# Kernel tuning notes

Hardware: AMD Instinct MI355X
Metric: run time of the kernel (lower is better)

The kernel has to match this reference:

```python
import jax, jax.numpy as jnp
import numpy as np

B, N, E, H, L = 1, 1024, 32, 1024, 8  # batch, num concepts, dim_edge, dim_hidden, stack_len


def setup_inputs() -> dict:
    key = jax.random.key(0)
    k = jax.random.split(key, 12)
    vision_feat = jax.random.normal(k[0], (B, 36, H), jnp.float32)   # unused by forward
    feat = jax.random.normal(k[1], (B, N - 1, N, E), jnp.float32)
    feat_edge = jax.random.normal(k[2], (B, 1, N, E), jnp.float32)
    c_i = jax.random.normal(k[3], (B, H), jnp.float32)
    relation_mask = jnp.ones((B, N), jnp.float32)                    # only its size is read
    att_stack = jax.random.uniform(k[4], (B, N, N, L), dtype=jnp.float32)
    sp = jax.random.uniform(k[5], (B, L), dtype=jnp.float32)
    stack_ptr = sp / jnp.sum(sp, axis=-1, keepdims=True)             # soft stack pointer
    mem_in = jax.random.normal(k[6], (B, H), jnp.float32)
    mono_mask = (jax.random.uniform(k[7], (B, N, N, 1)) > 0.5).astype(jnp.float32)
    cross_mask = jax.random.uniform(k[8], (E,), dtype=jnp.float32)
    w_c = jax.random.normal(k[9], (E, H), jnp.float32) / np.sqrt(H).astype(np.float32)
    b_c = jax.random.normal(k[10], (E,), jnp.float32) * 0.01
    return {"vision_feat": vision_feat, "feat": feat, "feat_edge": feat_edge,
            "c_i": c_i, "relation_mask": relation_mask, "att_stack": att_stack,
            "stack_ptr": stack_ptr, "mem_in": mem_in, "mono_mask": mono_mask,
            "cross_mask": cross_mask, "w_c": w_c, "b_c": b_c}


def reference(vision_feat, feat, feat_edge, c_i, relation_mask, att_stack,
              stack_ptr, mem_in, mono_mask, cross_mask, w_c, b_c):
    b = feat_edge.shape[0]
    # query = map_c(c_i).view(B,1,1,-1).expand_as(feat_edge)
    query = (c_i @ w_c.T + b_c).reshape(b, 1, 1, -1)
    query = jnp.broadcast_to(query, feat_edge.shape)                 # (B,1,N,E)
    I = jnp.concatenate([query, feat], axis=1)                       # (B,N,N,E)
    # Fusion: -(x-y)^2 + relu(x+y), feat_edge broadcasts over dim1
    elt_prod = -(I - feat_edge) ** 2 + jax.nn.relu(I + feat_edge)    # (B,N,N,E)
    weit_matrix = mono_mask * elt_prod                               # (B,N,N,E)
    # soft stack read + permute(0,2,1): att_in[b,y,x] = sum_l att_stack[b,x,y,l]*ptr[b,l]
    att_in = jnp.einsum('bxyl,bl->byx', att_stack, stack_ptr)        # (B,N,N)
    # (att_in @ weit_matrix) @ cross_mask, then permute(0,2,1).
    # Contract the edge dim first (mathematically identical by linearity).
    wv = jnp.einsum('bmye,e->bmy', weit_matrix, cross_mask)          # (B,N,N)
    att_out = jnp.einsum('bxy,bmy->bxm', att_in, wv)                 # (B,N,N)
    # max-normalize with detached norm clamped to >= 1
    norm = jax.lax.stop_gradient(jnp.max(att_out, axis=1, keepdims=True))
    norm = jnp.where(norm <= 1, jnp.ones_like(norm), norm)
    att_out = att_out / norm
    # soft stack write
    ptr = stack_ptr[:, None, None, :]                                # (B,1,1,L)
    att_stack_new = att_out[..., None] * ptr + att_stack * (1 - ptr) # (B,N,N,L)
    return att_stack_new, stack_ptr, jnp.zeros_like(mem_in)
```

## Files before the change

kernel.cpp:

```cpp
#include <hip/hip_runtime.h>
#include <math.h>

#define N 1024
#define E 32
#define L 8
#define NN ((size_t)N * N)

using short8 = __attribute__((ext_vector_type(8))) short;
using f32x4v = __attribute__((ext_vector_type(4))) float;

__device__ inline ushort2 split_bf16(float v) {
  unsigned ui = __float_as_uint(v);
  ushort h = (ushort)(ui >> 16);
  float hv = __uint_as_float((unsigned)h << 16);
  float r = v - hv;
  ushort l = (ushort)(__float_as_uint(r) >> 16);
  return make_ushort2(h, l);
}

__device__ inline void gload16(const void* g, void* l) {
  __builtin_amdgcn_global_load_lds(
      (const __attribute__((address_space(1))) unsigned int*)g,
      (__attribute__((address_space(3))) unsigned int*)l, 16, 0, 0);
}

__global__ __launch_bounds__(256) void k_wv(
    const float* __restrict__ feat, const float* __restrict__ fe,
    const float* __restrict__ mono, const float* __restrict__ cm,
    const float* __restrict__ c_i, const float* __restrict__ w_c,
    const float* __restrict__ b_c,
    ushort* __restrict__ wv_h, ushort* __restrict__ wv_l) {
  __shared__ __align__(16) float qsm[32];
  int tid = threadIdx.x;
  int b = blockIdx.x;
  int seg = tid & 7;
  int rl = tid >> 3;
  bool qblock = (b < 8);
  if (qblock) {
    int e = tid >> 3, r = tid & 7;
    float s = 0.f;
    for (int h = r; h < N; h += 8) s += c_i[h] * w_c[e * N + h];
    s += __shfl_down(s, 4, 8);
    s += __shfl_down(s, 2, 8);
    s += __shfl_down(s, 1, 8);
    if (r == 0) qsm[e] = s + b_c[e];
    __syncthreads();
  }
  float4 c = *(const float4*)(cm + seg * 4);
  float4 qa;
  if (qblock) qa = *((const float4*)qsm + seg);
  #pragma unroll
  for (int it = 0; it < 4; ++it) {
    int gid = b * 128 + it * 32 + rl;
    int m = gid >> 10;
    int y = gid & (N - 1);
    float4 a;
    if (qblock) {
      a = qa;
    } else {
      a = *(const float4*)(feat + ((size_t)(m - 1) * N + y) * E + seg * 4);
    }
    float4 f = *(const float4*)(fe + (size_t)y * E + seg * 4);
    float dx = a.x - f.x, dy = a.y - f.y, dz = a.z - f.z, dw = a.w - f.w;
    float s = c.x * (fmaxf(a.x + f.x, 0.f) - dx * dx)
            + c.y * (fmaxf(a.y + f.y, 0.f) - dy * dy)
            + c.z * (fmaxf(a.z + f.z, 0.f) - dz * dz)
            + c.w * (fmaxf(a.w + f.w, 0.f) - dw * dw);
    s += __shfl_down(s, 4, 8);
    s += __shfl_down(s, 2, 8);
    s += __shfl_down(s, 1, 8);
    if (seg == 0) {
      float v = mono[gid] * s;
      ushort2 hl = split_bf16(v);
      wv_h[gid] = hl.x;
      wv_l[gid] = hl.y;
    }
  }
}

__global__ __launch_bounds__(256) void k_P(
    const float* __restrict__ att_stack, const float* __restrict__ ptr,
    ushort* __restrict__ Pt_h, ushort* __restrict__ Pt_l,
    float* __restrict__ out_tail) {
  __shared__ ushort Ts[2][64][66];
  int tid = threadIdx.x;
  int b = blockIdx.x;
  if (b < 256) {
    int j0 = (b >> 4) * 64;
    int i0 = (b & 15) * 64;
    float p0 = ptr[0], p1 = ptr[1], p2 = ptr[2], p3 = ptr[3];
    float p4 = ptr[4], p5 = ptr[5], p6 = ptr[6], p7 = ptr[7];
    int w = tid >> 6, lane = tid & 63;
    #pragma unroll 4
    for (int r = 0; r < 16; ++r) {
      int jl = r * 4 + w;
      int il = lane;
      const float4* a =
          (const float4*)(att_stack + ((size_t)(j0 + jl) * N + i0 + il) * L);
      float4 a0 = a[0], a1 = a[1];
      float s = a0.x * p0 + a0.y * p1 + a0.z * p2 + a0.w * p3
              + a1.x * p4 + a1.y * p5 + a1.z * p6 + a1.w * p7;
      ushort2 hl = split_bf16(s);
      Ts[0][il][jl] = hl.x;
      Ts[1][il][jl] = hl.y;
    }
    __syncthreads();
    int il = tid >> 2, cc = tid & 3;
    size_t o = (size_t)(i0 + il) * N + j0 + cc * 16;
    {
      const uint* sp = (const uint*)&Ts[0][il][cc * 16];
      uint4 d0 = {sp[0], sp[1], sp[2], sp[3]};
      uint4 d1 = {sp[4], sp[5], sp[6], sp[7]};
      *(uint4*)&Pt_h[o] = d0;
      *(uint4*)&Pt_h[o + 8] = d1;
    }
    {
      const uint* sp = (const uint*)&Ts[1][il][cc * 16];
      uint4 d0 = {sp[0], sp[1], sp[2], sp[3]};
      uint4 d1 = {sp[4], sp[5], sp[6], sp[7]};
      *(uint4*)&Pt_l[o] = d0;
      *(uint4*)&Pt_l[o + 8] = d1;
    }
  } else {
    if (tid < 8) out_tail[tid] = ptr[tid];
    for (int i = tid; i < N; i += 256) out_tail[8 + i] = 0.f;
  }
}

__global__ __launch_bounds__(256) void k_mm(
    const ushort* __restrict__ Pt_h, const ushort* __restrict__ Pt_l,
    const ushort* __restrict__ wv_h, const ushort* __restrict__ wv_l,
    float* __restrict__ C, float* __restrict__ normp) {
  __shared__ ushort As[2][64][32];
  __shared__ ushort Bs[2][64][32];
  __shared__ float nm[64][17];
  int tid = threadIdx.x;
  int lane = tid & 63, w = tid >> 6;
  int x0 = blockIdx.x * 64, m0 = blockIdx.y * 64;
  int srow = w * 16 + (lane >> 2);
  int scol = (lane & 3) * 8;
  const ushort* gAh = Pt_h + (size_t)(x0 + srow) * N + scol;
  const ushort* gAl = Pt_l + (size_t)(x0 + srow) * N + scol;
  const ushort* gBh = wv_h + (size_t)(m0 + srow) * N + scol;
  const ushort* gBl = wv_l + (size_t)(m0 + srow) * N + scol;
  ushort* lAh = &As[0][w * 16][0];
  ushort* lAl = &As[1][w * 16][0];
  ushort* lBh = &Bs[0][w * 16][0];
  ushort* lBl = &Bs[1][w * 16][0];
  int fr = w * 16 + (lane & 15);
  int fk = (lane >> 4) * 8;
  int fn = lane & 15;
  f32x4v acc[4];
  #pragma unroll
  for (int t = 0; t < 4; ++t) acc[t] = (f32x4v){0.f, 0.f, 0.f, 0.f};
  for (int kt = 0; kt < 32; ++kt) {
    __syncthreads();
    gload16(gAh + kt * 32, lAh);
    gload16(gAl + kt * 32, lAl);
    gload16(gBh + kt * 32, lBh);
    gload16(gBl + kt * 32, lBl);
    __syncthreads();
    short8 Ah = *(const short8*)&As[0][fr][fk];
    short8 Al = *(const short8*)&As[1][fr][fk];
    #pragma unroll
    for (int t = 0; t < 4; ++t) {
      short8 Bh = *(const short8*)&Bs[0][t * 16 + fn][fk];
      short8 Bl = *(const short8*)&Bs[1][t * 16 + fn][fk];
      acc[t] = __builtin_amdgcn_mfma_f32_16x16x32_bf16(Ah, Bh, acc[t], 0, 0, 0);
      acc[t] = __builtin_amdgcn_mfma_f32_16x16x32_bf16(Ah, Bl, acc[t], 0, 0, 0);
      acc[t] = __builtin_amdgcn_mfma_f32_16x16x32_bf16(Al, Bh, acc[t], 0, 0, 0);
    }
  }
  int orow = x0 + w * 16 + (lane >> 4) * 4;
  int ocol = m0 + fn;
  int cidx = w * 4 + (lane >> 4);
  #pragma unroll
  for (int t = 0; t < 4; ++t) {
    float mx = -INFINITY;
    #pragma unroll
    for (int r = 0; r < 4; ++r) {
      float v = acc[t][r];
      C[(size_t)(orow + r) * N + ocol + t * 16] = v;
      mx = fmaxf(mx, v);
    }
    nm[t * 16 + fn][cidx] = mx;
  }
  __syncthreads();
  if (tid < 64) {
    float mx = nm[tid][0];
    #pragma unroll
    for (int j = 1; j < 16; ++j) mx = fmaxf(mx, nm[tid][j]);
    normp[(size_t)blockIdx.x * N + m0 + tid] = mx;
  }
}

__global__ __launch_bounds__(256) void k_norm2(
    const float* __restrict__ normp, float* __restrict__ norm) {
  int m = blockIdx.x * 256 + threadIdx.x;
  float mx = normp[m];
  #pragma unroll
  for (int xg = 1; xg < 16; ++xg)
    mx = fmaxf(mx, normp[(size_t)xg * N + m]);
  norm[m] = (mx <= 1.f) ? 1.f : mx;
}

__global__ __launch_bounds__(256) void k_blend(
    const float* __restrict__ C, const float* __restrict__ norm,
    const float* __restrict__ att_stack, const float* __restrict__ ptr,
    float* __restrict__ out) {
  int gid = blockIdx.x * 256 + threadIdx.x;
  int m = gid & (N - 1);
  float a = C[gid] / norm[m];
  const float4* s = (const float4*)(att_stack + (size_t)gid * L);
  float4 s0 = s[0], s1 = s[1];
  float p0 = ptr[0], p1 = ptr[1], p2 = ptr[2], p3 = ptr[3];
  float p4 = ptr[4], p5 = ptr[5], p6 = ptr[6], p7 = ptr[7];
  float4 o0, o1;
  o0.x = a * p0 + s0.x * (1.f - p0);
  o0.y = a * p1 + s0.y * (1.f - p1);
  o0.z = a * p2 + s0.z * (1.f - p2);
  o0.w = a * p3 + s0.w * (1.f - p3);
  o1.x = a * p4 + s1.x * (1.f - p4);
  o1.y = a * p5 + s1.y * (1.f - p5);
  o1.z = a * p6 + s1.z * (1.f - p6);
  o1.w = a * p7 + s1.w * (1.f - p7);
  float4* o = (float4*)(out + (size_t)gid * L);
  o[0] = o0;
  o[1] = o1;
}

extern "C" void kernel_launch(void* const* d_in, const int* in_sizes, int n_in,
                              void* d_out, int out_size, void* d_ws, size_t ws_size,
                              hipStream_t stream) {
  const float* feat      = (const float*)d_in[1];
  const float* feat_edge = (const float*)d_in[2];
  const float* c_i       = (const float*)d_in[3];
  const float* att_stack = (const float*)d_in[5];
  const float* stack_ptr = (const float*)d_in[6];
  const float* mono_mask = (const float*)d_in[8];
  const float* cross_mask= (const float*)d_in[9];
  const float* w_c       = (const float*)d_in[10];
  const float* b_c       = (const float*)d_in[11];

  float* out = (float*)d_out;

  ushort* wv_h = (ushort*)d_ws;
  ushort* wv_l = wv_h + NN;
  ushort* Pt_h = wv_l + NN;
  ushort* Pt_l = Pt_h + NN;
  float*  C    = (float*)(Pt_l + NN);
  float*  normp= C + NN;
  float*  norm = normp + (size_t)16 * N;

  float* out_tail = out + NN * L;

  k_wv<<<8192, 256, 0, stream>>>(feat, feat_edge, mono_mask, cross_mask,
                                 c_i, w_c, b_c, wv_h, wv_l);
  k_P<<<257, 256, 0, stream>>>(att_stack, stack_ptr, Pt_h, Pt_l, out_tail);
  dim3 mmgrid(16, 16);
  k_mm<<<mmgrid, 256, 0, stream>>>(Pt_h, Pt_l, wv_h, wv_l, C, normp);
  k_norm2<<<4, 256, 0, stream>>>(normp, norm);
  k_blend<<<4096, 256, 0, stream>>>(C, norm, att_stack, stack_ptr, out);
}
```

Before: 292.1 us.

## Merge prep kernels, double-buffer and swizzle GEMM LDS, fold norm into blend

Result: faster. 280.3 us (-4.0%).

```diff
diff --git a/kernel.cpp b/kernel.cpp
--- a/kernel.cpp
+++ b/kernel.cpp
@@ -24,70 +24,67 @@
       (__attribute__((address_space(3))) unsigned int*)l, 16, 0, 0);
 }
 
-__global__ __launch_bounds__(256) void k_wv(
+__global__ __launch_bounds__(256) void k_prep(
     const float* __restrict__ feat, const float* __restrict__ fe,
     const float* __restrict__ mono, const float* __restrict__ cm,
     const float* __restrict__ c_i, const float* __restrict__ w_c,
     const float* __restrict__ b_c,
-    ushort* __restrict__ wv_h, ushort* __restrict__ wv_l) {
-  __shared__ __align__(16) float qsm[32];
-  int tid = threadIdx.x;
-  int b = blockIdx.x;
-  int seg = tid & 7;
-  int rl = tid >> 3;
-  bool qblock = (b < 8);
-  if (qblock) {
-    int e = tid >> 3, r = tid & 7;
-    float s = 0.f;
-    for (int h = r; h < N; h += 8) s += c_i[h] * w_c[e * N + h];
-    s += __shfl_down(s, 4, 8);
-    s += __shfl_down(s, 2, 8);
-    s += __shfl_down(s, 1, 8);
-    if (r == 0) qsm[e] = s + b_c[e];
-    __syncthreads();
-  }
-  float4 c = *(const float4*)(cm + seg * 4);
-  float4 qa;
-  if (qblock) qa = *((const float4*)qsm + seg);
-  #pragma unroll
-  for (int it = 0; it < 4; ++it) {
-    int gid = b * 128 + it * 32 + rl;
-    int m = gid >> 10;
-    int y = gid & (N - 1);
-    float4 a;
-    if (qblock) {
-      a = qa;
-    } else {
-      a = *(const float4*)(feat + ((size_t)(m - 1) * N + y) * E + seg * 4);
-    }
-    float4 f = *(const float4*)(fe + (size_t)y * E + seg * 4);
-    float dx = a.x - f.x, dy = a.y - f.y, dz = a.z - f.z, dw = a.w - f.w;
-    float s = c.x * (fmaxf(a.x + f.x, 0.f) - dx * dx)
-            + c.y * (fmaxf(a.y + f.y, 0.f) - dy * dy)
-            + c.z * (fmaxf(a.z + f.z, 0.f) - dz * dz)
-            + c.w * (fmaxf(a.w + f.w, 0.f) - dw * dw);
-    s += __shfl_down(s, 4, 8);
-    s += __shfl_down(s, 2, 8);
-    s += __shfl_down(s, 1, 8);
-    if (seg == 0) {
-      float v = mono[gid] * s;
-      ushort2 hl = split_bf16(v);
-      wv_h[gid] = hl.x;
-      wv_l[gid] = hl.y;
-    }
-  }
-}
-
-__global__ __launch_bounds__(256) void k_P(
     const float* __restrict__ att_stack, const float* __restrict__ ptr,
+    ushort* __restrict__ wv_h, ushort* __restrict__ wv_l,
     ushort* __restrict__ Pt_h, ushort* __restrict__ Pt_l,
     float* __restrict__ out_tail) {
+  __shared__ __align__(16) float qsm[32];
   __shared__ ushort Ts[2][64][66];
   int tid = threadIdx.x;
   int b = blockIdx.x;
-  if (b < 256) {
-    int j0 = (b >> 4) * 64;
-    int i0 = (b & 15) * 64;
+  if (b < 8192) {
+    int seg = tid & 7;
+    int rl = tid >> 3;
+    bool qblock = (b < 8);
+    if (qblock) {
+      int e = tid >> 3, r = tid & 7;
+      float s = 0.f;
+      for (int h = r; h < N; h += 8) s += c_i[h] * w_c[e * N + h];
+      s += __shfl_down(s, 4, 8);
+      s += __shfl_down(s, 2, 8);
+      s += __shfl_down(s, 1, 8);
+      if (r == 0) qsm[e] = s + b_c[e];
+      __syncthreads();
+    }
+    float4 c = *(const float4*)(cm + seg * 4);
+    float4 qa;
+    if (qblock) qa = *((const float4*)qsm + seg);
+    #pragma unroll
+    for (int it = 0; it < 4; ++it) {
+      int gid = b * 128 + it * 32 + rl;
+      int m = gid >> 10;
+      int y = gid & (N - 1);
+      float4 a;
+      if (qblock) {
+        a = qa;
+      } else {
+        a = *(const float4*)(feat + ((size_t)(m - 1) * N + y) * E + seg * 4);
+      }
+      float4 f = *(const float4*)(fe + (size_t)y * E + seg * 4);
+      float dx = a.x - f.x, dy = a.y - f.y, dz = a.z - f.z, dw = a.w - f.w;
+      float s = c.x * (fmaxf(a.x + f.x, 0.f) - dx * dx)
+              + c.y * (fmaxf(a.y + f.y, 0.f) - dy * dy)
+              + c.z * (fmaxf(a.z + f.z, 0.f) - dz * dz)
+              + c.w * (fmaxf(a.w + f.w, 0.f) - dw * dw);
+      s += __shfl_down(s, 4, 8);
+      s += __shfl_down(s, 2, 8);
+      s += __shfl_down(s, 1, 8);
+      if (seg == 0) {
+        float v = mono[gid] * s;
+        ushort2 hl = split_bf16(v);
+        wv_h[gid] = hl.x;
+        wv_l[gid] = hl.y;
+      }
+    }
+  } else if (b < 8448) {
+    int b2 = b - 8192;
+    int j0 = (b2 >> 4) * 64;
+    int i0 = (b2 & 15) * 64;
     float p0 = ptr[0], p1 = ptr[1], p2 = ptr[2], p3 = ptr[3];
     float p4 = ptr[4], p5 = ptr[5], p6 = ptr[6], p7 = ptr[7];
     int w = tid >> 6, lane = tid & 63;
@@ -131,41 +128,49 @@
     const ushort* __restrict__ Pt_h, const ushort* __restrict__ Pt_l,
     const ushort* __restrict__ wv_h, const ushort* __restrict__ wv_l,
     float* __restrict__ C, float* __restrict__ normp) {
-  __shared__ ushort As[2][64][32];
-  __shared__ ushort Bs[2][64][32];
+  __shared__ ushort As[2][2][64][32];
+  __shared__ ushort Bs[2][2][64][32];
   __shared__ float nm[64][17];
   int tid = threadIdx.x;
   int lane = tid & 63, w = tid >> 6;
   int x0 = blockIdx.x * 64, m0 = blockIdx.y * 64;
   int srow = w * 16 + (lane >> 2);
-  int scol = (lane & 3) * 8;
-  const ushort* gAh = Pt_h + (size_t)(x0 + srow) * N + scol;
-  const ushort* gAl = Pt_l + (size_t)(x0 + srow) * N + scol;
-  const ushort* gBh = wv_h + (size_t)(m0 + srow) * N + scol;
-  const ushort* gBl = wv_l + (size_t)(m0 + srow) * N + scol;
-  ushort* lAh = &As[0][w * 16][0];
-  ushort* lAl = &As[1][w * 16][0];
-  ushort* lBh = &Bs[0][w * 16][0];
-  ushort* lBl = &Bs[1][w * 16][0];
+  int gsrc = (((lane & 3) ^ ((lane >> 3) & 3))) * 8;
+  const ushort* gAh = Pt_h + (size_t)(x0 + srow) * N + gsrc;
+  const ushort* gAl = Pt_l + (size_t)(x0 + srow) * N + gsrc;
+  const ushort* gBh = wv_h + (size_t)(m0 + srow) * N + gsrc;
+  const ushort* gBl = wv_l + (size_t)(m0 + srow) * N + gsrc;
   int fr = w * 16 + (lane & 15);
-  int fk = (lane >> 4) * 8;
   int fn = lane & 15;
+  int grn = ((lane >> 4) ^ ((lane >> 1) & 3)) << 4;
   f32x4v acc[4];
   #pragma unroll
   for (int t = 0; t < 4; ++t) acc[t] = (f32x4v){0.f, 0.f, 0.f, 0.f};
+  gload16(gAh, &As[0][0][w * 16][0]);
+  gload16(gAl, &As[0][1][w * 16][0]);
+  gload16(gBh, &Bs[0][0][w * 16][0]);
+  gload16(gBl, &Bs[0][1][w * 16][0]);
+  #pragma unroll 2
   for (int kt = 0; kt < 32; ++kt) {
+    int cur = kt & 1;
     __syncthreads();
-    gload16(gAh + kt * 32, lAh);
-    gload16(gAl + kt * 32, lAl);
-    gload16(gBh + kt * 32, lBh);
-    gload16(gBl + kt * 32, lBl);
-    __syncthreads();
-    short8 Ah = *(const short8*)&As[0][fr][fk];
-    short8 Al = *(const short8*)&As[1][fr][fk];
+    if (kt < 31) {
+      int nxt = cur ^ 1;
+      gload16(gAh + (kt + 1) * 32, &As[nxt][0][w * 16][0]);
+      gload16(gAl + (kt + 1) * 32, &As[nxt][1][w * 16][0]);
+      gload16(gBh + (kt + 1) * 32, &Bs[nxt][0][w * 16][0]);
+      gload16(gBl + (kt + 1) * 32, &Bs[nxt][1][w * 16][0]);
+    }
+    const char* aB0 = (const char*)&As[cur][0][0][0];
+    const char* aB1 = (const char*)&As[cur][1][0][0];
+    short8 Ah = *(const short8*)(aB0 + fr * 64 + grn);
+    short8 Al = *(const short8*)(aB1 + fr * 64 + grn);
+    const char* bB0 = (const char*)&Bs[cur][0][0][0];
+    const char* bB1 = (const char*)&Bs[cur][1][0][0];
     #pragma unroll
     for (int t = 0; t < 4; ++t) {
-      short8 Bh = *(const short8*)&Bs[0][t * 16 + fn][fk];
-      short8 Bl = *(const short8*)&Bs[1][t * 16 + fn][fk];
+      short8 Bh = *(const short8*)(bB0 + (t * 16 + fn) * 64 + grn);
+      short8 Bl = *(const short8*)(bB1 + (t * 16 + fn) * 64 + grn);
       acc[t] = __builtin_amdgcn_mfma_f32_16x16x32_bf16(Ah, Bh, acc[t], 0, 0, 0);
       acc[t] = __builtin_amdgcn_mfma_f32_16x16x32_bf16(Ah, Bl, acc[t], 0, 0, 0);
       acc[t] = __builtin_amdgcn_mfma_f32_16x16x32_bf16(Al, Bh, acc[t], 0, 0, 0);
@@ -194,23 +199,18 @@
   }
 }
 
-__global__ __launch_bounds__(256) void k_norm2(
-    const float* __restrict__ normp, float* __restrict__ norm) {
-  int m = blockIdx.x * 256 + threadIdx.x;
+__global__ __launch_bounds__(256) void k_fin(
+    const float* __restrict__ C, const float* __restrict__ normp,
+    const float* __restrict__ att_stack, const float* __restrict__ ptr,
+    float* __restrict__ out) {
+  int gid = blockIdx.x * 256 + threadIdx.x;
+  int m = gid & (N - 1);
   float mx = normp[m];
   #pragma unroll
   for (int xg = 1; xg < 16; ++xg)
     mx = fmaxf(mx, normp[(size_t)xg * N + m]);
-  norm[m] = (mx <= 1.f) ? 1.f : mx;
-}
-
-__global__ __launch_bounds__(256) void k_blend(
-    const float* __restrict__ C, const float* __restrict__ norm,
-    const float* __restrict__ att_stack, const float* __restrict__ ptr,
-    float* __restrict__ out) {
-  int gid = blockIdx.x * 256 + threadIdx.x;
-  int m = gid & (N - 1);
-  float a = C[gid] / norm[m];
+  float nrm = (mx <= 1.f) ? 1.f : mx;
+  float a = C[gid] / nrm;
   const float4* s = (const float4*)(att_stack + (size_t)gid * L);
   float4 s0 = s[0], s1 = s[1];
   float p0 = ptr[0], p1 = ptr[1], p2 = ptr[2], p3 = ptr[3];
@@ -250,15 +250,13 @@
   ushort* Pt_l = Pt_h + NN;
   float*  C    = (float*)(Pt_l + NN);
   float*  normp= C + NN;
-  float*  norm = normp + (size_t)16 * N;
 
   float* out_tail = out + NN * L;
 
-  k_wv<<<8192, 256, 0, stream>>>(feat, feat_edge, mono_mask, cross_mask,
-                                 c_i, w_c, b_c, wv_h, wv_l);
-  k_P<<<257, 256, 0, stream>>>(att_stack, stack_ptr, Pt_h, Pt_l, out_tail);
+  k_prep<<<8449, 256, 0, stream>>>(feat, feat_edge, mono_mask, cross_mask,
+                                   c_i, w_c, b_c, att_stack, stack_ptr,
+                                   wv_h, wv_l, Pt_h, Pt_l, out_tail);
   dim3 mmgrid(16, 16);
   k_mm<<<mmgrid, 256, 0, stream>>>(Pt_h, Pt_l, wv_h, wv_l, C, normp);
-  k_norm2<<<4, 256, 0, stream>>>(normp, norm);
-  k_blend<<<4096, 256, 0, stream>>>(C, norm, att_stack, stack_ptr, out);
-}
+  k_fin<<<4096, 256, 0, stream>>>(C, normp, att_stack, stack_ptr, out);
+}
```
